# Optimization experiments

Measured on AMD Instinct MI355X. Metric: run time of the kernel, lower is better.

Reference implementation:

```python
import jax, jax.numpy as jnp
import numpy as np

N = 100000   # nodes
H = 96       # hidden_dim
A = 32       # attn_dim
De = 16      # edge_embeddings_dim
E = 500000   # edges per edge type
NEG_SLOPE = 0.01  # torch F.leaky_relu default


def setup_inputs() -> dict:
    key = jax.random.key(0)
    ks = jax.random.split(key, 24)
    nrm = lambda k, shape, s=1.0: jax.random.normal(k, shape, dtype=jnp.float32) * s
    idx = lambda k: jax.random.randint(k, (E,), 0, N, dtype=jnp.int32)
    Din = 2 * H + De
    return {
        'h': nrm(ks[0], (N, H)),
        'src0': idx(ks[1]), 'dst0': idx(ks[2]),
        'src1': idx(ks[3]), 'dst1': idx(ks[4]),
        'src2': idx(ks[5]), 'dst2': idx(ks[6]),
        'Wm0': nrm(ks[7], (Din, H), Din ** -0.5), 'bm0': jnp.zeros((H,), jnp.float32), 'ef0': nrm(ks[8], (De,)),
        'Wm1': nrm(ks[9], (Din, H), Din ** -0.5), 'bm1': jnp.zeros((H,), jnp.float32), 'ef1': nrm(ks[10], (De,)),
        'Wm2': nrm(ks[11], (Din, H), Din ** -0.5), 'bm2': jnp.zeros((H,), jnp.float32), 'ef2': nrm(ks[12], (De,)),
        'Wn0': nrm(ks[13], (H, A), H ** -0.5), 'Wa0': nrm(ks[14], (2 * A, 1), (2 * A) ** -0.5),
        'Wn1': nrm(ks[15], (H, A), H ** -0.5), 'Wa1': nrm(ks[16], (2 * A, 1), (2 * A) ** -0.5),
        'Wu': nrm(ks[17], (4 * H, H), (4 * H) ** -0.5), 'bu': jnp.zeros((H,), jnp.float32),
    }


def _leaky(x):
    return jnp.where(x > 0, x, NEG_SLOPE * x)


def _edge_msg(h, src, dst, Wm, bm, ef):
    # cat(src_h, dst_h, edge_feature) -> Linear  (dropout p=0, eval mode)
    x = jnp.concatenate([h[src], h[dst], jnp.broadcast_to(ef, (src.shape[0], ef.shape[0]))], axis=-1)
    return x @ Wm + bm  # [E, H]


def _mean_agg(m, dst):
    # fn.mean('m','msg'): per-destination mean over incoming edges
    s = jax.ops.segment_sum(m, dst, num_segments=N)
    c = jax.ops.segment_sum(jnp.ones((m.shape[0],), m.dtype), dst, num_segments=N)
    return s / jnp.maximum(c, 1.0)[:, None]


def _attn_agg(scores, m, dst):
    # per-destination softmax over mailbox (variable-size), then weighted sum
    smax = jax.ops.segment_max(scores, dst, num_segments=N)
    ex = jnp.exp(scores - smax[dst])
    den = jax.ops.segment_sum(ex, dst, num_segments=N)
    num = jax.ops.segment_sum(ex[:, None] * m, dst, num_segments=N)
    return num / jnp.maximum(den, 1e-9)[:, None]


def reference(h, src0, dst0, src1, dst1, src2, dst2,
              Wm0, bm0, ef0, Wm1, bm1, ef1, Wm2, bm2, ef2,
              Wn0, Wa0, Wn1, Wa1, Wu, bu):
    # edge type 0: intra_diff (attention), type 1: inter_diff (attention), type 2: intra_lt (mean)
    m0 = _edge_msg(h, src0, dst0, Wm0, bm0, ef0)
    m1 = _edge_msg(h, src1, dst1, Wm1, bm1, ef1)
    m2 = _edge_msg(h, src2, dst2, Wm2, bm2, ef2)

    z0 = h @ Wn0  # [N, A]
    s0 = _leaky(jnp.concatenate([z0[src0], z0[dst0]], axis=-1) @ Wa0)[:, 0]  # [E]
    z1 = h @ Wn1
    s1 = _leaky(jnp.concatenate([z1[src1], z1[dst1]], axis=-1) @ Wa1)[:, 0]

    msg0 = _attn_agg(s0, m0, dst0)   # [N, H]
    msg1 = _attn_agg(s1, m1, dst1)
    msg2 = _mean_agg(m2, dst2)

    # cross_reducer='stack' then concat over edge-type dim -> [N, 3H]
    mcat = jnp.concatenate([msg0, msg1, msg2], axis=-1)
    # cell node update: Linear(cat(h, m)) + ReLU
    return jax.nn.relu(jnp.concatenate([h, mcat], axis=-1) @ Wu + bu)
```

## Files before the change

### kernel.cpp

```cpp
#include <hip/hip_runtime.h>
#include <hip/hip_bf16.h>
#include <cstdint>

#define NN 100000
#define HH 96
#define AD 32
#define DE 16
#define EE 500000
#define NEG 0.01f

#define GSH 10
#define GSZ 1024
#define KB 98
#define CH 4096
#define BPT 123

typedef __bf16 bf16x8 __attribute__((ext_vector_type(8)));
typedef float  f32x4  __attribute__((ext_vector_type(4)));

__device__ __forceinline__ unsigned short f2b(float x) {
    union { float f; unsigned int u; } v; v.f = x;
    unsigned int r = v.u + 0x7fffu + ((v.u >> 16) & 1u);
    return (unsigned short)(r >> 16);
}
__device__ __forceinline__ float b2f(unsigned short h) {
    union { unsigned int u; float f; } v; v.u = ((unsigned int)h) << 16;
    return v.f;
}

__global__ void prep_kernel(const float* Wm0, const float* bm0, const float* ef0,
                            const float* Wm1, const float* bm1, const float* ef1,
                            const float* Wm2, const float* bm2, const float* ef2,
                            const float* Wn0, const float* Wa0,
                            const float* Wn1, const float* Wa1,
                            const float* Wu,
                            float* cvec, float* wvec,
                            unsigned short* BfN, unsigned short* BfU) {
    const float* Wm[3] = {Wm0, Wm1, Wm2};
    const float* bm[3] = {bm0, bm1, bm2};
    const float* ef[3] = {ef0, ef1, ef2};
    const int total = 288 + 384 + 55296 + 36864;
    for (int i = blockIdx.x * blockDim.x + threadIdx.x; i < total;
         i += gridDim.x * blockDim.x) {
        if (i < 288) {
            int t = i / 96, j = i % 96;
            float s = bm[t][j];
            for (int k = 0; k < DE; ++k) s += ef[t][k] * Wm[t][(2 * HH + k) * HH + j];
            cvec[i] = s;
        } else if (i < 288 + 384) {
            int ii = i - 288;
            int kind = ii / 96, k = ii % 96;
            const float* Wn = (kind < 2) ? Wn0 : Wn1;
            const float* Wa = (kind < 2) ? Wa0 : Wa1;
            int off = (kind & 1) ? AD : 0;
            float s = 0.f;
            for (int a = 0; a < AD; ++a) s += Wn[k * AD + a] * Wa[off + a];
            wvec[ii] = s;
        } else if (i < 288 + 384 + 55296) {
            int ii = i - 672;
            int sec = ii / 9216; int rem = ii % 9216;
            int ksc = rem / 512; int lj = rem % 512;
            int ks = ksc / 6, c = ksc % 6;
            int lane = lj / 8, jj = lj % 8;
            int quad = lane / 16, m = lane % 16;
            int k = ks * 32 + quad * 8 + jj;
            int n = c * 16 + m;
            int mt = (sec < 3) ? sec : sec - 3;
            int rowoff = (sec < 3) ? 0 : HH;
            BfN[ii] = f2b(Wm[mt][(rowoff + k) * HH + n]);
        } else {
            int ii = i - (672 + 55296);
            int ksc = ii / 512; int lj = ii % 512;
            int ks = ksc / 6, c = ksc % 6;
            int lane = lj / 8, jj = lj % 8;
            int quad = lane / 16, m = lane % 16;
            int k = ks * 32 + quad * 8 + jj;
            int n = c * 16 + m;
            BfU[ii] = f2b(Wu[k * HH + n]);
        }
    }
}

__global__ void cast_uv_kernel(const float* __restrict__ h, const float* __restrict__ wvec,
                               unsigned short* __restrict__ hb, float* __restrict__ uv) {
    int lane = threadIdx.x & 31;
    int node = (blockIdx.x * blockDim.x + threadIdx.x) >> 5;
    if (node >= NN) return;
    float h0 = h[node * HH + lane];
    float h1 = h[node * HH + 32 + lane];
    float h2 = h[node * HH + 64 + lane];
    hb[node * HH + lane] = f2b(h0);
    hb[node * HH + 32 + lane] = f2b(h1);
    hb[node * HH + 64 + lane] = f2b(h2);
    float acc[4];
#pragma unroll
    for (int q = 0; q < 4; ++q)
        acc[q] = h0 * wvec[q * 96 + lane] + h1 * wvec[q * 96 + 32 + lane] +
                 h2 * wvec[q * 96 + 64 + lane];
#pragma unroll
    for (int d = 16; d >= 1; d >>= 1)
#pragma unroll
        for (int q = 0; q < 4; ++q) acc[q] += __shfl_down(acc[q], d, 32);
    if (lane == 0) {
#pragma unroll
        for (int q = 0; q < 4; ++q) uv[q * NN + node] = acc[q];
    }
}

__global__ void zero_kernel(float4* __restrict__ p, int n4) {
    for (int i = blockIdx.x * blockDim.x + threadIdx.x; i < n4;
         i += gridDim.x * blockDim.x)
        p[i] = make_float4(0.f, 0.f, 0.f, 0.f);
}

__global__ void bucket_hist(const int* __restrict__ d0, const int* __restrict__ d1,
                            const int* __restrict__ d2, int* __restrict__ bCnt) {
    __shared__ int hist[3 * KB];
    int t = threadIdx.x;
    for (int j = t; j < 3 * KB; j += 256) hist[j] = 0;
    __syncthreads();
    const int total = 3 * EE;
    for (int i = blockIdx.x * blockDim.x + t; i < total; i += gridDim.x * blockDim.x) {
        int ty = i / EE, e = i - ty * EE;
        const int* d = (ty == 0) ? d0 : (ty == 1) ? d1 : d2;
        atomicAdd(&hist[ty * KB + (d[e] >> GSH)], 1);
    }
    __syncthreads();
    for (int j = t; j < 3 * KB; j += 256)
        if (hist[j]) atomicAdd(&bCnt[j], hist[j]);
}

__global__ void bucket_scan(const int* __restrict__ bCnt, int* __restrict__ bBase,
                            int* __restrict__ gCursor, int* __restrict__ rs) {
    __shared__ int hist[3 * KB];
    int t = threadIdx.x;
    if (t < 3 * KB) hist[t] = bCnt[t];
    __syncthreads();
    if (t < 3) {
        int run = 0;
        for (int b = 0; b < KB; ++b) {
            bBase[t * (KB + 1) + b] = run;
            gCursor[t * KB + b] = run;
            run += hist[t * KB + b];
        }
        bBase[t * (KB + 1) + KB] = run;
        rs[(size_t)t * (NN + 1) + NN] = run;
    }
}

__global__ __launch_bounds__(256) void bucket_scatter(
    const int* __restrict__ s0, const int* __restrict__ d0,
    const int* __restrict__ s1, const int* __restrict__ d1,
    const int* __restrict__ s2, const int* __restrict__ d2,
    int* __restrict__ gCursor, unsigned int* __restrict__ binned) {
    __shared__ unsigned int recs[CH];
    __shared__ unsigned short rnk[CH];
    __shared__ unsigned char bkt[CH];
    __shared__ int cnt[KB];
    __shared__ int gpos[KB];
    int t = threadIdx.x;
    int type = blockIdx.x / BPT;
    int chunk = (blockIdx.x % BPT) * CH;
    const int* src = (type == 0) ? s0 : (type == 1) ? s1 : s2;
    const int* dst = (type == 0) ? d0 : (type == 1) ? d1 : d2;
    if (t < KB) cnt[t] = 0;
    __syncthreads();
#pragma unroll
    for (int k = 0; k < CH / 256; ++k) {
        int idx = k * 256 + t;
        int e = chunk + idx;
        if (e < EE) {
            int s = src[e], d = dst[e];
            int b = d >> GSH;
            recs[idx] = ((unsigned int)s << GSH) | (unsigned int)(d & (GSZ - 1));
            bkt[idx] = (unsigned char)b;
            rnk[idx] = (unsigned short)atomicAdd(&cnt[b], 1);
        } else {
            bkt[idx] = 0xFF;
        }
    }
    __syncthreads();
    if (t < KB) {
        int c = cnt[t];
        gpos[t] = (c > 0) ? atomicAdd(&gCursor[type * KB + t], c) : 0;
    }
    __syncthreads();
    unsigned int* bout = binned + (size_t)type * EE;
#pragma unroll
    for (int k = 0; k < CH / 256; ++k) {
        int idx = k * 256 + t;
        unsigned char b = bkt[idx];
        if (b != 0xFF) bout[gpos[b] + rnk[idx]] = recs[idx];
    }
}

__global__ __launch_bounds__(256) void bucket_sort(
    const unsigned int* __restrict__ binned, const int* __restrict__ bBase,
    int* __restrict__ rs, int* __restrict__ sorted) {
    __shared__ int cnt[GSZ];
    __shared__ int tsum[256];
    int t = threadIdx.x;
    int type = blockIdx.x / KB;
    int b = blockIdx.x % KB;
    int nodeBase = b * GSZ;
    int eb = bBase[type * (KB + 1) + b];
    int en = bBase[type * (KB + 1) + b + 1];
    int n = en - eb;
    const unsigned int* bin = binned + (size_t)type * EE + eb;
#pragma unroll
    for (int k = 0; k < GSZ / 256; ++k) cnt[k * 256 + t] = 0;
    __syncthreads();
    for (int i = t; i < n; i += 256) atomicAdd(&cnt[bin[i] & (GSZ - 1)], 1);
    __syncthreads();
    int v[4], s = 0;
#pragma unroll
    for (int k = 0; k < 4; ++k) { v[k] = cnt[t * 4 + k]; s += v[k]; }
    tsum[t] = s;
    __syncthreads();
    for (int off = 1; off < 256; off <<= 1) {
        int add = (t >= off) ? tsum[t - off] : 0;
        __syncthreads();
        tsum[t] += add;
        __syncthreads();
    }
    int run = tsum[t] - s;
    int offk[4];
#pragma unroll
    for (int k = 0; k < 4; ++k) { offk[k] = run; run += v[k]; }
    int* rsrow = rs + (size_t)type * (NN + 1) + nodeBase;
#pragma unroll
    for (int k = 0; k < 4; ++k) {
        int node = t * 4 + k;
        if (nodeBase + node < NN) rsrow[node] = eb + offk[k];
    }
    __syncthreads();
#pragma unroll
    for (int k = 0; k < 4; ++k) cnt[t * 4 + k] = offk[k];
    __syncthreads();
    int* so = sorted + (size_t)type * EE + eb;
    for (int i = t; i < n; i += 256) {
        unsigned int r = bin[i];
        int dl = r & (GSZ - 1);
        int p = atomicAdd(&cnt[dl], 1);
        so[p] = (int)(r >> GSH);
    }
}

__global__ __launch_bounds__(256) void node_gemm_kernel(const unsigned short* __restrict__ hb,
                                                        const unsigned short* __restrict__ BfN,
                                                        int t,
                                                        unsigned short* __restrict__ Pb,
                                                        unsigned short* __restrict__ Qb) {
    int wave = threadIdx.x >> 6;
    int lane = threadIdx.x & 63;
    int quad = lane >> 4, m = lane & 15;
    int blk = blockIdx.x * 4 + wave;
    if (blk >= NN / 16) return;
    int sec = t + 3 * blockIdx.y;
    unsigned short* dst = blockIdx.y ? Qb : Pb;
    int r0 = blk * 16;
    f32x4 acc[6] = {};
    const unsigned short* arow = hb + (size_t)(r0 + m) * HH + quad * 8;
#pragma unroll
    for (int ks = 0; ks < 3; ++ks) {
        bf16x8 af = *(const bf16x8*)(arow + ks * 32);
#pragma unroll
        for (int c = 0; c < 6; ++c) {
            bf16x8 bfv = *(const bf16x8*)(BfN + (((sec * 3 + ks) * 6 + c) << 9) + lane * 8);
            acc[c] = __builtin_amdgcn_mfma_f32_16x16x32_bf16(af, bfv, acc[c], 0, 0, 0);
        }
    }
#pragma unroll
    for (int c = 0; c < 6; ++c)
#pragma unroll
        for (int r = 0; r < 4; ++r) {
            int row = r0 + quad * 4 + r;
            dst[(size_t)row * HH + c * 16 + m] = f2b(acc[c][r]);
        }
}

__global__ void aggregate_kernel(const int* __restrict__ rs, const int* __restrict__ sorted,
                                 const float* __restrict__ u, const float* __restrict__ vv,
                                 const unsigned short* __restrict__ P,
                                 const unsigned short* __restrict__ Q,
                                 const float* __restrict__ cvec_t, int is_attn,
                                 unsigned short* __restrict__ msgb_t) {
    int lane = threadIdx.x & 31;
    int node = (blockIdx.x * blockDim.x + threadIdx.x) >> 5;
    if (node >= NN) return;
    int beg = rs[node], end = rs[node + 1];
    float a0 = 0.f, a1 = 0.f, a2 = 0.f, den = 0.f;
    float vd = is_attn ? vv[node] : 0.f;
    for (int base = beg; base < end; base += 32) {
        int batch = end - base;
        if (batch > 32) batch = 32;
        int li = lane < batch ? lane : batch - 1;
        int myS = sorted[base + li];
#pragma unroll 1
        for (int j = 0; j < batch; j += 4) {
            int rem = batch - j;
            int s0 = __shfl(myS, j, 32);
            int s1 = __shfl(myS, rem > 1 ? j + 1 : j, 32);
            int s2 = __shfl(myS, rem > 2 ? j + 2 : j, 32);
            int s3 = __shfl(myS, rem > 3 ? j + 3 : j, 32);
            float w0, w1, w2, w3;
            if (is_attn) {
                float c0 = u[s0] + vd, c1 = u[s1] + vd, c2 = u[s2] + vd, c3 = u[s3] + vd;
                c0 = c0 > 0.f ? c0 : NEG * c0;
                c1 = c1 > 0.f ? c1 : NEG * c1;
                c2 = c2 > 0.f ? c2 : NEG * c2;
                c3 = c3 > 0.f ? c3 : NEG * c3;
                w0 = __expf(c0); w1 = __expf(c1); w2 = __expf(c2); w3 = __expf(c3);
            } else {
                w0 = w1 = w2 = w3 = 1.f;
            }
            if (rem < 4) { w3 = 0.f; if (rem < 3) { w2 = 0.f; if (rem < 2) w1 = 0.f; } }
            const unsigned short* p0 = P + (size_t)s0 * HH;
            const unsigned short* p1 = P + (size_t)s1 * HH;
            const unsigned short* p2 = P + (size_t)s2 * HH;
            const unsigned short* p3 = P + (size_t)s3 * HH;
            float x00 = b2f(p0[lane]),      x01 = b2f(p0[lane + 32]), x02 = b2f(p0[lane + 64]);
            float x10 = b2f(p1[lane]),      x11 = b2f(p1[lane + 32]), x12 = b2f(p1[lane + 64]);
            float x20 = b2f(p2[lane]),      x21 = b2f(p2[lane + 32]), x22 = b2f(p2[lane + 64]);
            float x30 = b2f(p3[lane]),      x31 = b2f(p3[lane + 32]), x32 = b2f(p3[lane + 64]);
            den += w0 + w1 + w2 + w3;
            a0 += w0 * x00 + w1 * x10 + w2 * x20 + w3 * x30;
            a1 += w0 * x01 + w1 * x11 + w2 * x21 + w3 * x31;
            a2 += w0 * x02 + w1 * x12 + w2 * x22 + w3 * x32;
        }
    }
    float r0 = 0.f, r1 = 0.f, r2 = 0.f;
    if (den > 0.f) {
        float inv = 1.f / den;
        const unsigned short* qr = Q + (size_t)node * HH;
        r0 = a0 * inv + b2f(qr[lane]) + cvec_t[lane];
        r1 = a1 * inv + b2f(qr[lane + 32]) + cvec_t[lane + 32];
        r2 = a2 * inv + b2f(qr[lane + 64]) + cvec_t[lane + 64];
    }
    unsigned short* mr = msgb_t + (size_t)node * 288;
    mr[lane] = f2b(r0);
    mr[lane + 32] = f2b(r1);
    mr[lane + 64] = f2b(r2);
}

__global__ __launch_bounds__(256) void update_gemm_kernel(const unsigned short* __restrict__ hb,
                                                          const unsigned short* __restrict__ msgb,
                                                          const unsigned short* __restrict__ BfU,
                                                          const float* __restrict__ bu,
                                                          float* __restrict__ out) {
    int wave = threadIdx.x >> 6;
    int lane = threadIdx.x & 63;
    int quad = lane >> 4, m = lane & 15;
    int blk = blockIdx.x * 4 + wave;
    if (blk >= NN / 16) return;
    int r0 = blk * 16;
    f32x4 acc[6] = {};
#pragma unroll
    for (int ks = 0; ks < 12; ++ks) {
        const unsigned short* ap =
            (ks < 3) ? hb + (size_t)(r0 + m) * HH + ks * 32 + quad * 8
                     : msgb + (size_t)(r0 + m) * 288 + (ks - 3) * 32 + quad * 8;
        bf16x8 af = *(const bf16x8*)ap;
#pragma unroll
        for (int c = 0; c < 6; ++c) {
            bf16x8 bfv = *(const bf16x8*)(BfU + ((ks * 6 + c) << 9) + lane * 8);
            acc[c] = __builtin_amdgcn_mfma_f32_16x16x32_bf16(af, bfv, acc[c], 0, 0, 0);
        }
    }
#pragma unroll
    for (int c = 0; c < 6; ++c) {
        float b = bu[c * 16 + m];
#pragma unroll
        for (int r = 0; r < 4; ++r) {
            int row = r0 + quad * 4 + r;
            float v2 = acc[c][r] + b;
            out[(size_t)row * HH + c * 16 + m] = v2 > 0.f ? v2 : 0.f;
        }
    }
}

extern "C" void kernel_launch(void* const* d_in, const int* in_sizes, int n_in,
                              void* d_out, int out_size, void* d_ws, size_t ws_size,
                              hipStream_t stream) {
    (void)in_sizes; (void)n_in; (void)out_size;
    const float* h   = (const float*)d_in[0];
    const int* srcs[3] = {(const int*)d_in[1], (const int*)d_in[3], (const int*)d_in[5]};
    const int* dsts[3] = {(const int*)d_in[2], (const int*)d_in[4], (const int*)d_in[6]};
    const float* Wm0 = (const float*)d_in[7];
    const float* bm0 = (const float*)d_in[8];
    const float* ef0 = (const float*)d_in[9];
    const float* Wm1 = (const float*)d_in[10];
    const float* bm1 = (const float*)d_in[11];
    const float* ef1 = (const float*)d_in[12];
    const float* Wm2 = (const float*)d_in[13];
    const float* bm2 = (const float*)d_in[14];
    const float* ef2 = (const float*)d_in[15];
    const float* Wn0 = (const float*)d_in[16];
    const float* Wa0 = (const float*)d_in[17];
    const float* Wn1 = (const float*)d_in[18];
    const float* Wa1 = (const float*)d_in[19];
    const float* Wu  = (const float*)d_in[20];
    const float* bu  = (const float*)d_in[21];
    float* out = (float*)d_out;

    const size_t NEED = 130191104;
    if (ws_size < NEED) return;
    char* w = (char*)d_ws;
    unsigned short* msgb    = (unsigned short*)(w + 0);
    unsigned short* hb      = (unsigned short*)(w + 57600000);
    unsigned short* Pb      = (unsigned short*)(w + 76800000);
    unsigned short* Qb      = (unsigned short*)(w + 96000000);
    float*          uv      = (float*)(w + 115200000);
    float*          cvec    = (float*)(w + 116800000);
    float*          wvec    = (float*)(w + 116801280);
    unsigned short* BfN     = (unsigned short*)(w + 116802816);
    unsigned short* BfU     = (unsigned short*)(w + 116913408);
    int*            bBase   = (int*)(w + 116987136);
    int*            gCursor = (int*)(w + 116988416);
    int*            bCnt    = (int*)(w + 116989696);
    int*            rs      = (int*)(w + 116990976);
    int*            sorted  = (int*)(w + 118191104);
    unsigned int*   binned  = (unsigned int*)(w + 124191104);

    prep_kernel<<<128, 256, 0, stream>>>(Wm0, bm0, ef0, Wm1, bm1, ef1, Wm2, bm2, ef2,
                                         Wn0, Wa0, Wn1, Wa1, Wu, cvec, wvec, BfN, BfU);
    cast_uv_kernel<<<12500, 256, 0, stream>>>(h, wvec, hb, uv);

    zero_kernel<<<1, 256, 0, stream>>>((float4*)bCnt, 80);
    bucket_hist<<<512, 256, 0, stream>>>(dsts[0], dsts[1], dsts[2], bCnt);
    bucket_scan<<<1, 384, 0, stream>>>(bCnt, bBase, gCursor, rs);
    bucket_scatter<<<3 * BPT, 256, 0, stream>>>(srcs[0], dsts[0], srcs[1], dsts[1],
                                                srcs[2], dsts[2], gCursor, binned);
    bucket_sort<<<3 * KB, 256, 0, stream>>>(binned, bBase, rs, sorted);

    for (int t = 0; t < 3; ++t) {
        node_gemm_kernel<<<dim3(1563, 2), 256, 0, stream>>>(hb, BfN, t, Pb, Qb);
        aggregate_kernel<<<12500, 256, 0, stream>>>(rs + t * (NN + 1), sorted + t * EE,
                                                    uv + 2 * t * NN, uv + (2 * t + 1) * NN,
                                                    Pb, Qb, cvec + t * 96, (t < 2) ? 1 : 0,
                                                    msgb + t * 96);
    }

    update_gemm_kernel<<<1563, 256, 0, stream>>>(hb, msgb, BfU, bu, out);
}
```

Baseline: 363.3 us.

## Batch per-edge-type GEMM and aggregation into single launches, gather 8 rows per step

The three per-edge-type node GEMM and aggregate launches are merged into one launch each, with the edge type taken from blockIdx.y. P and Q now get separate buffers per type, which enlarges the workspace. This removes four launches and the serialization between types, so all types run concurrently on more blocks. The aggregation inner loop also gathers 8 source rows per iteration instead of 4 to raise memory-level parallelism, at the cost of more registers and more cache pressure from the larger working set.

```diff
diff --git a/kernel.cpp b/kernel.cpp
--- a/kernel.cpp
+++ b/kernel.cpp
@@ -248,16 +248,17 @@
 
 __global__ __launch_bounds__(256) void node_gemm_kernel(const unsigned short* __restrict__ hb,
                                                         const unsigned short* __restrict__ BfN,
-                                                        int t,
-                                                        unsigned short* __restrict__ Pb,
-                                                        unsigned short* __restrict__ Qb) {
+                                                        unsigned short* __restrict__ Pall,
+                                                        unsigned short* __restrict__ Qall) {
+    const size_t NH = (size_t)NN * HH;
     int wave = threadIdx.x >> 6;
     int lane = threadIdx.x & 63;
     int quad = lane >> 4, m = lane & 15;
     int blk = blockIdx.x * 4 + wave;
     if (blk >= NN / 16) return;
-    int sec = t + 3 * blockIdx.y;
-    unsigned short* dst = blockIdx.y ? Qb : Pb;
+    int sec = blockIdx.y;
+    unsigned short* dst = (sec < 3) ? (Pall + (size_t)sec * NH)
+                                    : (Qall + (size_t)(sec - 3) * NH);
     int r0 = blk * 16;
     f32x4 acc[6] = {};
     const unsigned short* arow = hb + (size_t)(r0 + m) * HH + quad * 8;
@@ -279,54 +280,68 @@
         }
 }
 
-__global__ void aggregate_kernel(const int* __restrict__ rs, const int* __restrict__ sorted,
-                                 const float* __restrict__ u, const float* __restrict__ vv,
-                                 const unsigned short* __restrict__ P,
-                                 const unsigned short* __restrict__ Q,
-                                 const float* __restrict__ cvec_t, int is_attn,
-                                 unsigned short* __restrict__ msgb_t) {
+__global__ void aggregate_kernel(const int* __restrict__ rsAll, const int* __restrict__ sortedAll,
+                                 const float* __restrict__ uv,
+                                 const unsigned short* __restrict__ Pall,
+                                 const unsigned short* __restrict__ Qall,
+                                 const float* __restrict__ cvec,
+                                 unsigned short* __restrict__ msgb) {
+    const size_t NH = (size_t)NN * HH;
     int lane = threadIdx.x & 31;
     int node = (blockIdx.x * blockDim.x + threadIdx.x) >> 5;
     if (node >= NN) return;
+    int t = blockIdx.y;
+    int is_attn = (t < 2);
+    const int* rs = rsAll + (size_t)t * (NN + 1);
+    const int* sorted = sortedAll + (size_t)t * EE;
+    const float* u = uv + 2 * t * NN;
+    const unsigned short* P = Pall + (size_t)t * NH;
+    const unsigned short* Q = Qall + (size_t)t * NH;
+    const float* cvec_t = cvec + t * 96;
+
     int beg = rs[node], end = rs[node + 1];
     float a0 = 0.f, a1 = 0.f, a2 = 0.f, den = 0.f;
-    float vd = is_attn ? vv[node] : 0.f;
+    float vd = is_attn ? uv[(2 * t + 1) * NN + node] : 0.f;
     for (int base = beg; base < end; base += 32) {
         int batch = end - base;
         if (batch > 32) batch = 32;
         int li = lane < batch ? lane : batch - 1;
         int myS = sorted[base + li];
 #pragma unroll 1
-        for (int j = 0; j < batch; j += 4) {
+        for (int j = 0; j < batch; j += 8) {
             int rem = batch - j;
-            int s0 = __shfl(myS, j, 32);
-            int s1 = __shfl(myS, rem > 1 ? j + 1 : j, 32);
-            int s2 = __shfl(myS, rem > 2 ? j + 2 : j, 32);
-            int s3 = __shfl(myS, rem > 3 ? j + 3 : j, 32);
-            float w0, w1, w2, w3;
+            int sI[8];
+            float wv[8];
+#pragma unroll
+            for (int k = 0; k < 8; ++k) sI[k] = __shfl(myS, (k < rem ? j + k : j), 32);
             if (is_attn) {
-                float c0 = u[s0] + vd, c1 = u[s1] + vd, c2 = u[s2] + vd, c3 = u[s3] + vd;
-                c0 = c0 > 0.f ? c0 : NEG * c0;
-                c1 = c1 > 0.f ? c1 : NEG * c1;
-                c2 = c2 > 0.f ? c2 : NEG * c2;
-                c3 = c3 > 0.f ? c3 : NEG * c3;
-                w0 = __expf(c0); w1 = __expf(c1); w2 = __expf(c2); w3 = __expf(c3);
+#pragma unroll
+                for (int k = 0; k < 8; ++k) {
+                    float c = u[sI[k]] + vd;
+                    c = c > 0.f ? c : NEG * c;
+                    wv[k] = __expf(c);
+                }
             } else {
-                w0 = w1 = w2 = w3 = 1.f;
+#pragma unroll
+                for (int k = 0; k < 8; ++k) wv[k] = 1.f;
             }
-            if (rem < 4) { w3 = 0.f; if (rem < 3) { w2 = 0.f; if (rem < 2) w1 = 0.f; } }
-            const unsigned short* p0 = P + (size_t)s0 * HH;
-            const unsigned short* p1 = P + (size_t)s1 * HH;
-            const unsigned short* p2 = P + (size_t)s2 * HH;
-            const unsigned short* p3 = P + (size_t)s3 * HH;
-            float x00 = b2f(p0[lane]),      x01 = b2f(p0[lane + 32]), x02 = b2f(p0[lane + 64]);
-            float x10 = b2f(p1[lane]),      x11 = b2f(p1[lane + 32]), x12 = b2f(p1[lane + 64]);
-            float x20 = b2f(p2[lane]),      x21 = b2f(p2[lane + 32]), x22 = b2f(p2[lane + 64]);
-            float x30 = b2f(p3[lane]),      x31 = b2f(p3[lane + 32]), x32 = b2f(p3[lane + 64]);
-            den += w0 + w1 + w2 + w3;
-            a0 += w0 * x00 + w1 * x10 + w2 * x20 + w3 * x30;
-            a1 += w0 * x01 + w1 * x11 + w2 * x21 + w3 * x31;
-            a2 += w0 * x02 + w1 * x12 + w2 * x22 + w3 * x32;
+#pragma unroll
+            for (int k = 0; k < 8; ++k) if (k >= rem) wv[k] = 0.f;
+            float x0[8], x1[8], x2[8];
+#pragma unroll
+            for (int k = 0; k < 8; ++k) {
+                const unsigned short* pr = P + (size_t)sI[k] * HH;
+                x0[k] = b2f(pr[lane]);
+                x1[k] = b2f(pr[lane + 32]);
+                x2[k] = b2f(pr[lane + 64]);
+            }
+#pragma unroll
+            for (int k = 0; k < 8; ++k) {
+                den += wv[k];
+                a0 += wv[k] * x0[k];
+                a1 += wv[k] * x1[k];
+                a2 += wv[k] * x2[k];
+            }
         }
     }
     float r0 = 0.f, r1 = 0.f, r2 = 0.f;
@@ -337,7 +352,7 @@
         r1 = a1 * inv + b2f(qr[lane + 32]) + cvec_t[lane + 32];
         r2 = a2 * inv + b2f(qr[lane + 64]) + cvec_t[lane + 64];
     }
-    unsigned short* mr = msgb_t + (size_t)node * 288;
+    unsigned short* mr = msgb + (size_t)node * 288 + t * 96;
     mr[lane] = f2b(r0);
     mr[lane + 32] = f2b(r1);
     mr[lane + 64] = f2b(r2);
@@ -403,24 +418,24 @@
     const float* bu  = (const float*)d_in[21];
     float* out = (float*)d_out;
 
-    const size_t NEED = 130191104;
+    const size_t NEED = 206991104;
     if (ws_size < NEED) return;
     char* w = (char*)d_ws;
     unsigned short* msgb    = (unsigned short*)(w + 0);
     unsigned short* hb      = (unsigned short*)(w + 57600000);
-    unsigned short* Pb      = (unsigned short*)(w + 76800000);
-    unsigned short* Qb      = (unsigned short*)(w + 96000000);
-    float*          uv      = (float*)(w + 115200000);
-    float*          cvec    = (float*)(w + 116800000);
-    float*          wvec    = (float*)(w + 116801280);
-    unsigned short* BfN     = (unsigned short*)(w + 116802816);
-    unsigned short* BfU     = (unsigned short*)(w + 116913408);
-    int*            bBase   = (int*)(w + 116987136);
-    int*            gCursor = (int*)(w + 116988416);
-    int*            bCnt    = (int*)(w + 116989696);
-    int*            rs      = (int*)(w + 116990976);
-    int*            sorted  = (int*)(w + 118191104);
-    unsigned int*   binned  = (unsigned int*)(w + 124191104);
+    unsigned short* Pall    = (unsigned short*)(w + 76800000);
+    unsigned short* Qall    = (unsigned short*)(w + 134400000);
+    float*          uv      = (float*)(w + 192000000);
+    float*          cvec    = (float*)(w + 193600000);
+    float*          wvec    = (float*)(w + 193601280);
+    unsigned short* BfN     = (unsigned short*)(w + 193602816);
+    unsigned short* BfU     = (unsigned short*)(w + 193713408);
+    int*            bBase   = (int*)(w + 193787136);
+    int*            gCursor = (int*)(w + 193788416);
+    int*            bCnt    = (int*)(w + 193789696);
+    int*            rs      = (int*)(w + 193790976);
+    int*            sorted  = (int*)(w + 194991104);
+    unsigned int*   binned  = (unsigned int*)(w + 200991104);
 
     prep_kernel<<<128, 256, 0, stream>>>(Wm0, bm0, ef0, Wm1, bm1, ef1, Wm2, bm2, ef2,
                                          Wn0, Wa0, Wn1, Wa1, Wu, cvec, wvec, BfN, BfU);
@@ -433,13 +448,8 @@
                                                 srcs[2], dsts[2], gCursor, binned);
     bucket_sort<<<3 * KB, 256, 0, stream>>>(binned, bBase, rs, sorted);
 
-    for (int t = 0; t < 3; ++t) {
-        node_gemm_kernel<<<dim3(1563, 2), 256, 0, stream>>>(hb, BfN, t, Pb, Qb);
-        aggregate_kernel<<<12500, 256, 0, stream>>>(rs + t * (NN + 1), sorted + t * EE,
-                                                    uv + 2 * t * NN, uv + (2 * t + 1) * NN,
-                                                    Pb, Qb, cvec + t * 96, (t < 2) ? 1 : 0,
-                                                    msgb + t * 96);
-    }
-
+    node_gemm_kernel<<<dim3(1563, 6), 256, 0, stream>>>(hb, BfN, Pall, Qall);
+    aggregate_kernel<<<dim3(12500, 3), 256, 0, stream>>>(rs, sorted, uv, Pall, Qall,
+                                                         cvec, msgb);
     update_gemm_kernel<<<1563, 256, 0, stream>>>(hb, msgb, BfU, bu, out);
 }
```

Result: faster. 346.9 us (-4.5%).
